# Kernel tuning notes

Hardware: AMD Instinct MI355X
Metric: run time of the kernel (lower is better)

Reference implementation:

```python
import jax, jax.numpy as jnp
import numpy as np

BASIS_SIZE = 256          # levels of the bitfield code
R_MAX = 1.0               # quantization range for normalized weights
QMAX = BASIS_SIZE // 2 - 1  # 127 -> symmetric int8-style grid
EPS = 1e-8


def setup_inputs() -> dict:
    key = jax.random.key(0)
    kx, kw, kb = jax.random.split(key, 3)
    B, S, D_IN, D_OUT = 4, 2048, 4096, 4096
    x = jax.random.normal(kx, (B, S, D_IN), dtype=jnp.float32)
    W = jax.random.normal(kw, (D_OUT, D_IN), dtype=jnp.float32)
    bias = jax.random.normal(kb, (D_OUT,), dtype=jnp.float32)
    return {"x": x, "W": W, "bias": bias}


def _bitfield_dequant_weight(W):
    # per-output-row L2 norm (p=2, dim=1 in torch)
    weight_norms = jnp.sqrt(jnp.sum(W * W, axis=1))          # [out]
    W_normalized = W / (weight_norms[:, None] + EPS)          # rows ~unit norm
    # bitfield encode/decode: uniform symmetric quantization to BASIS_SIZE
    # levels in [-R_MAX, R_MAX]
    scale = R_MAX / QMAX
    Wq = jnp.round(jnp.clip(W_normalized, -R_MAX, R_MAX) / scale) * scale
    return Wq, weight_norms


def reference(x, W, bias):
    Wq, weight_norms = _bitfield_dequant_weight(W)
    B, S, D_IN = x.shape
    x2 = x.reshape(-1, D_IN)                                  # [B*S, in]
    # bitfield matmul on normalized weights
    out_norm = jnp.einsum('nd,od->no', x2, Wq)                # [B*S, out]
    # denormalize (restore row norms) + bias epilogue
    out = out_norm * weight_norms
    out = out.reshape(B, S, -1) + bias
    return out
```

## Files before the change

### kernel.cpp

```cpp
#include <hip/hip_runtime.h>
#include <hip/hip_bf16.h>

typedef __attribute__((ext_vector_type(4))) int i32x4;
typedef __attribute__((address_space(3))) char lds3;

#define D_IN  4096
#define D_OUT 4096
#define M_TOT 8192
#define RSTRIDE ((size_t)64 * D_IN)

__device__ __forceinline__ void async16(const void* g, lds3* l) {
  __builtin_amdgcn_global_load_lds(
      (__attribute__((address_space(1))) void*)g,
      (__attribute__((address_space(3))) void*)l,
      16, 0, 0);
}

#define DSR(dst, addr, off) \
  asm volatile("ds_read_b128 %0, %1 offset:%2" : "=v"(dst) : "v"(addr), "i"(off))

__device__ __forceinline__ int pack4(float a, float b, float c, float d, float s) {
  int q0 = (int)rintf(a * s) & 255;
  int q1 = (int)rintf(b * s) & 255;
  int q2 = (int)rintf(c * s) & 255;
  int q3 = (int)rintf(d * s) & 255;
  return q0 | (q1 << 8) | (q2 << 16) | (q3 << 24);
}

__global__ void quant_x_kernel(const float* __restrict__ x, int4* __restrict__ xq,
                               float* __restrict__ sx) {
  const int row = blockIdx.x;
  const int t = threadIdx.x;
  const float* xr = x + (size_t)row * D_IN;

  float4 v[4];
  float mx = 0.f;
#pragma unroll
  for (int j = 0; j < 4; j++) {
    v[j] = ((const float4*)xr)[t * 4 + j];
    mx = fmaxf(mx, fmaxf(fmaxf(fabsf(v[j].x), fabsf(v[j].y)),
                         fmaxf(fabsf(v[j].z), fabsf(v[j].w))));
  }
#pragma unroll
  for (int off = 32; off; off >>= 1) mx = fmaxf(mx, __shfl_down(mx, off));
  __shared__ float red[4];
  __shared__ float smx;
  if ((t & 63) == 0) red[t >> 6] = mx;
  __syncthreads();
  if (t == 0) {
    float m = fmaxf(fmaxf(red[0], red[1]), fmaxf(red[2], red[3]));
    smx = m;
    sx[row] = m * (1.0f / 127.0f);
  }
  __syncthreads();

  const float inv = 127.0f / smx;
  int4 o;
  o.x = pack4(v[0].x, v[0].y, v[0].z, v[0].w, inv);
  o.y = pack4(v[1].x, v[1].y, v[1].z, v[1].w, inv);
  o.z = pack4(v[2].x, v[2].y, v[2].z, v[2].w, inv);
  o.w = pack4(v[3].x, v[3].y, v[3].z, v[3].w, inv);
  xq[(size_t)row * (D_IN / 16) + t] = o;
}

__global__ void quant_w_kernel(const float* __restrict__ W, int4* __restrict__ wq,
                               float* __restrict__ sn) {
  const int row = blockIdx.x;
  const int t = threadIdx.x;
  const float* wr = W + (size_t)row * D_IN;

  float4 v[4];
  double ss = 0.0;
#pragma unroll
  for (int j = 0; j < 4; j++) {
    v[j] = ((const float4*)wr)[t * 4 + j];
    ss += (double)v[j].x * v[j].x + (double)v[j].y * v[j].y +
          (double)v[j].z * v[j].z + (double)v[j].w * v[j].w;
  }
#pragma unroll
  for (int off = 32; off; off >>= 1) ss += __shfl_down(ss, off);
  __shared__ double red[4];
  __shared__ float shn;
  if ((t & 63) == 0) red[t >> 6] = ss;
  __syncthreads();
  if (t == 0) {
    double tot = red[0] + red[1] + red[2] + red[3];
    float nrm = (float)sqrt(tot);
    shn = nrm;
    sn[row] = nrm * (1.0f / 127.0f);
  }
  __syncthreads();

  const float den = shn + 1e-8f;
  int4 o;
  int* op = (int*)&o;
#pragma unroll
  for (int j = 0; j < 4; j++) {
    float e[4] = {v[j].x, v[j].y, v[j].z, v[j].w};
    int q[4];
#pragma unroll
    for (int c = 0; c < 4; c++) {
      float wn = e[c] / den;
      wn = fminf(1.0f, fmaxf(-1.0f, wn));
      q[c] = (int)rintf(wn * 127.0f) & 255;
    }
    op[j] = q[0] | (q[1] << 8) | (q[2] << 16) | (q[3] << 24);
  }
  wq[(size_t)row * (D_IN / 16) + t] = o;
}

template<int S, int VM, bool ISSUE>
__device__ __forceinline__ void k_iter(unsigned aA, unsigned aB,
                                       const char* pA, const char* pB,
                                       lds3* lA, lds3* lB,
                                       i32x4 (&acc)[4][4]) {
  asm volatile("s_waitcnt vmcnt(%0)" :: "i"(VM));
  asm volatile("s_barrier" ::: "memory");
  if (ISSUE) {
    async16(pA, lA);
    async16(pA + RSTRIDE, lA + 4096);
    async16(pB, lB);
    async16(pB + RSTRIDE, lB + 4096);
  }
  i32x4 af[4], bf[4];
  DSR(af[0], aA, S * 16384 + 0);
  DSR(af[1], aA, S * 16384 + 1024);
  DSR(af[2], aA, S * 16384 + 2048);
  DSR(af[3], aA, S * 16384 + 3072);
  DSR(bf[0], aB, S * 16384 + 8192 + 0);
  DSR(bf[1], aB, S * 16384 + 8192 + 1024);
  DSR(bf[2], aB, S * 16384 + 8192 + 2048);
  DSR(bf[3], aB, S * 16384 + 8192 + 3072);
  asm volatile("s_waitcnt lgkmcnt(0)"
               : "+v"(af[0]), "+v"(af[1]), "+v"(af[2]), "+v"(af[3]),
                 "+v"(bf[0]), "+v"(bf[1]), "+v"(bf[2]), "+v"(bf[3]));
#pragma unroll
  for (int mi = 0; mi < 4; mi++)
#pragma unroll
    for (int ni = 0; ni < 4; ni++)
      acc[mi][ni] = __builtin_amdgcn_mfma_i32_16x16x64_i8(af[mi], bf[ni], acc[mi][ni], 0, 0, 0);
}

__global__ __launch_bounds__(256, 3)
void gemm_i8_kernel(const char* __restrict__ A, const char* __restrict__ B,
                    const float* __restrict__ sx, const float* __restrict__ sn,
                    const float* __restrict__ bias, float* __restrict__ C) {
  __shared__ __align__(16) char smem[3 * 16384];

  const int t = threadIdx.x;
  const int lane = t & 63;
  const int wave = t >> 6;
  const int wm = wave >> 1, wn = wave & 1;
  const int m0 = blockIdx.y * 128;
  const int n0 = blockIdx.x * 128;

  const int srow = t >> 2;
  const int q = ((t & 3) - ((srow & 15) >> 1)) & 3;
  const char* gA = A + (size_t)(m0 + srow) * D_IN + q * 16;
  const char* gB = B + (size_t)(n0 + srow) * D_IN + q * 16;

  lds3* l3 = (lds3*)smem;
  lds3* lA0 = l3 + t * 16;
  lds3* lB0 = l3 + 8192 + t * 16;

  const int ml = lane & 15;
  const int g = lane >> 4;
  const unsigned cperm = (unsigned)((g + (ml >> 1)) & 3);
  const unsigned lds_base = (unsigned)(size_t)l3;
  const unsigned aA = lds_base + (wm * 64 + ml) * 64 + cperm * 16;
  const unsigned aB = lds_base + (wn * 64 + ml) * 64 + cperm * 16;

  i32x4 acc[4][4];
#pragma unroll
  for (int i = 0; i < 4; i++)
#pragma unroll
    for (int j = 0; j < 4; j++) acc[i][j] = (i32x4)0;

  async16(gA, lA0);            async16(gA + RSTRIDE, lA0 + 4096);
  async16(gB, lB0);            async16(gB + RSTRIDE, lB0 + 4096);
  async16(gA + 64, lA0 + 16384);           async16(gA + 64 + RSTRIDE, lA0 + 16384 + 4096);
  async16(gB + 64, lB0 + 16384);           async16(gB + 64 + RSTRIDE, lB0 + 16384 + 4096);

  const char* pA = gA + 128;
  const char* pB = gB + 128;

#pragma unroll 1
  for (int tr = 0; tr < 20; ++tr) {
    k_iter<0, 4, true>(aA, aB, pA, pB, lA0 + 32768, lB0 + 32768, acc); pA += 64; pB += 64;
    k_iter<1, 4, true>(aA, aB, pA, pB, lA0,         lB0,         acc); pA += 64; pB += 64;
    k_iter<2, 4, true>(aA, aB, pA, pB, lA0 + 16384, lB0 + 16384, acc); pA += 64; pB += 64;
  }
  k_iter<0, 4, true >(aA, aB, pA, pB, lA0 + 32768, lB0 + 32768, acc); pA += 64; pB += 64;
  k_iter<1, 4, true >(aA, aB, pA, pB, lA0,         lB0,         acc);
  k_iter<2, 4, false>(aA, aB, pA, pB, lA0,         lB0,         acc);
  k_iter<0, 0, false>(aA, aB, pA, pB, lA0,         lB0,         acc);

  float scn[4], bsv[4];
#pragma unroll
  for (int ni = 0; ni < 4; ni++) {
    const int col = n0 + wn * 64 + ni * 16 + ml;
    scn[ni] = sn[col];
    bsv[ni] = bias[col];
  }
#pragma unroll
  for (int mi = 0; mi < 4; mi++) {
    const int rbase = m0 + wm * 64 + mi * 16 + g * 4;
    float sxv[4];
#pragma unroll
    for (int r = 0; r < 4; r++) sxv[r] = sx[rbase + r];
#pragma unroll
    for (int ni = 0; ni < 4; ni++) {
      const int col = n0 + wn * 64 + ni * 16 + ml;
#pragma unroll
      for (int r = 0; r < 4; r++)
        C[(size_t)(rbase + r) * D_OUT + col] =
            (float)acc[mi][ni][r] * (sxv[r] * scn[ni]) + bsv[ni];
    }
  }
}

extern "C" void kernel_launch(void* const* d_in, const int* in_sizes, int n_in,
                              void* d_out, int out_size, void* d_ws, size_t ws_size,
                              hipStream_t stream) {
  const float* x    = (const float*)d_in[0];
  const float* W    = (const float*)d_in[1];
  const float* bias = (const float*)d_in[2];
  float* out = (float*)d_out;

  char* ws = (char*)d_ws;
  char*  xq = ws;
  char*  wq = ws + (size_t)M_TOT * D_IN;
  float* sx = (float*)(wq + (size_t)D_OUT * D_IN);
  float* sn = sx + M_TOT;

  quant_x_kernel<<<M_TOT, 256, 0, stream>>>(x, (int4*)xq, sx);
  quant_w_kernel<<<D_OUT, 256, 0, stream>>>(W, (int4*)wq, sn);
  dim3 grid(D_OUT / 128, M_TOT / 128);
  gemm_i8_kernel<<<grid, 256, 0, stream>>>(xq, wq, sx, sn, bias, out);
}
```

Baseline: 406.2 us.

## Software-pipeline LDS fragment reads with MFMA and use one wave per quant row

The int8 GEMM main loop now double-buffers register fragments. LDS reads for the next k-slice are issued before the MFMAs for the current slice, with sched_barriers and setprio used to keep that order and raise MFMA priority. This aims to hide ds_read latency behind the matrix cores, at the cost of more VGPRs, which may pressure occupancy under launch_bounds(256,3). The quantization kernels now give each 64-lane wave one row with coalesced loads and a shuffle-only reduction, removing the shared memory and __syncthreads barriers.

```diff
diff --git a/kernel.cpp b/kernel.cpp
--- a/kernel.cpp
+++ b/kernel.cpp
@@ -27,75 +27,54 @@
   return q0 | (q1 << 8) | (q2 << 16) | (q3 << 24);
 }
 
-__global__ void quant_x_kernel(const float* __restrict__ x, int4* __restrict__ xq,
+__global__ void quant_x_kernel(const float* __restrict__ x, int* __restrict__ xq,
                                float* __restrict__ sx) {
-  const int row = blockIdx.x;
-  const int t = threadIdx.x;
-  const float* xr = x + (size_t)row * D_IN;
-
-  float4 v[4];
+  const int row = blockIdx.x * 4 + (threadIdx.x >> 6);
+  const int lane = threadIdx.x & 63;
+  const float4* xr = (const float4*)(x + (size_t)row * D_IN);
+
+  float4 v[16];
   float mx = 0.f;
 #pragma unroll
-  for (int j = 0; j < 4; j++) {
-    v[j] = ((const float4*)xr)[t * 4 + j];
+  for (int j = 0; j < 16; j++) {
+    v[j] = xr[j * 64 + lane];
     mx = fmaxf(mx, fmaxf(fmaxf(fabsf(v[j].x), fabsf(v[j].y)),
                          fmaxf(fabsf(v[j].z), fabsf(v[j].w))));
   }
 #pragma unroll
-  for (int off = 32; off; off >>= 1) mx = fmaxf(mx, __shfl_down(mx, off));
-  __shared__ float red[4];
-  __shared__ float smx;
-  if ((t & 63) == 0) red[t >> 6] = mx;
-  __syncthreads();
-  if (t == 0) {
-    float m = fmaxf(fmaxf(red[0], red[1]), fmaxf(red[2], red[3]));
-    smx = m;
-    sx[row] = m * (1.0f / 127.0f);
-  }
-  __syncthreads();
-
-  const float inv = 127.0f / smx;
-  int4 o;
-  o.x = pack4(v[0].x, v[0].y, v[0].z, v[0].w, inv);
-  o.y = pack4(v[1].x, v[1].y, v[1].z, v[1].w, inv);
-  o.z = pack4(v[2].x, v[2].y, v[2].z, v[2].w, inv);
-  o.w = pack4(v[3].x, v[3].y, v[3].z, v[3].w, inv);
-  xq[(size_t)row * (D_IN / 16) + t] = o;
-}
-
-__global__ void quant_w_kernel(const float* __restrict__ W, int4* __restrict__ wq,
+  for (int off = 32; off; off >>= 1) mx = fmaxf(mx, __shfl_xor(mx, off));
+  if (lane == 0) sx[row] = mx * (1.0f / 127.0f);
+
+  const float inv = 127.0f / mx;
+  int* xqr = xq + (size_t)row * (D_IN / 4);
+#pragma unroll
+  for (int j = 0; j < 16; j++)
+    xqr[j * 64 + lane] = pack4(v[j].x, v[j].y, v[j].z, v[j].w, inv);
+}
+
+__global__ void quant_w_kernel(const float* __restrict__ W, int* __restrict__ wq,
                                float* __restrict__ sn) {
-  const int row = blockIdx.x;
-  const int t = threadIdx.x;
-  const float* wr = W + (size_t)row * D_IN;
-
-  float4 v[4];
+  const int row = blockIdx.x * 4 + (threadIdx.x >> 6);
+  const int lane = threadIdx.x & 63;
+  const float4* wr = (const float4*)(W + (size_t)row * D_IN);
+
+  float4 v[16];
   double ss = 0.0;
 #pragma unroll
-  for (int j = 0; j < 4; j++) {
-    v[j] = ((const float4*)wr)[t * 4 + j];
+  for (int j = 0; j < 16; j++) {
+    v[j] = wr[j * 64 + lane];
     ss += (double)v[j].x * v[j].x + (double)v[j].y * v[j].y +
           (double)v[j].z * v[j].z + (double)v[j].w * v[j].w;
   }
 #pragma unroll
-  for (int off = 32; off; off >>= 1) ss += __shfl_down(ss, off);
-  __shared__ double red[4];
-  __shared__ float shn;
-  if ((t & 63) == 0) red[t >> 6] = ss;
-  __syncthreads();
-  if (t == 0) {
-    double tot = red[0] + red[1] + red[2] + red[3];
-    float nrm = (float)sqrt(tot);
-    shn = nrm;
-    sn[row] = nrm * (1.0f / 127.0f);
-  }
-  __syncthreads();
-
-  const float den = shn + 1e-8f;
-  int4 o;
-  int* op = (int*)&o;
-#pragma unroll
-  for (int j = 0; j < 4; j++) {
+  for (int off = 32; off; off >>= 1) ss += __shfl_xor(ss, off);
+  const float nrm = (float)sqrt(ss);
+  if (lane == 0) sn[row] = nrm * (1.0f / 127.0f);
+
+  const float den = nrm + 1e-8f;
+  int* wqr = wq + (size_t)row * (D_IN / 4);
+#pragma unroll
+  for (int j = 0; j < 16; j++) {
     float e[4] = {v[j].x, v[j].y, v[j].z, v[j].w};
     int q[4];
 #pragma unroll
@@ -104,41 +83,47 @@
       wn = fminf(1.0f, fmaxf(-1.0f, wn));
       q[c] = (int)rintf(wn * 127.0f) & 255;
     }
-    op[j] = q[0] | (q[1] << 8) | (q[2] << 16) | (q[3] << 24);
-  }
-  wq[(size_t)row * (D_IN / 16) + t] = o;
-}
-
-template<int S, int VM, bool ISSUE>
-__device__ __forceinline__ void k_iter(unsigned aA, unsigned aB,
-                                       const char* pA, const char* pB,
-                                       lds3* lA, lds3* lB,
+    wqr[j * 64 + lane] = q[0] | (q[1] << 8) | (q[2] << 16) | (q[3] << 24);
+  }
+}
+
+template<int S, int VM, bool ISSUE, bool MF>
+__device__ __forceinline__ void k_pipe(unsigned aA, unsigned aB,
+                                       const char*& pA, const char*& pB,
+                                       lds3* lA0, lds3* lB0,
+                                       i32x4 (&fill)[8], i32x4 (&use)[8],
                                        i32x4 (&acc)[4][4]) {
   asm volatile("s_waitcnt vmcnt(%0)" :: "i"(VM));
   asm volatile("s_barrier" ::: "memory");
   if (ISSUE) {
-    async16(pA, lA);
-    async16(pA + RSTRIDE, lA + 4096);
-    async16(pB, lB);
-    async16(pB + RSTRIDE, lB + 4096);
-  }
-  i32x4 af[4], bf[4];
-  DSR(af[0], aA, S * 16384 + 0);
-  DSR(af[1], aA, S * 16384 + 1024);
-  DSR(af[2], aA, S * 16384 + 2048);
-  DSR(af[3], aA, S * 16384 + 3072);
-  DSR(bf[0], aB, S * 16384 + 8192 + 0);
-  DSR(bf[1], aB, S * 16384 + 8192 + 1024);
-  DSR(bf[2], aB, S * 16384 + 8192 + 2048);
-  DSR(bf[3], aB, S * 16384 + 8192 + 3072);
+    constexpr int T = ((S + 2) % 3) * 16384;
+    async16(pA, lA0 + T);  async16(pA + RSTRIDE, lA0 + T + 4096);
+    async16(pB, lB0 + T);  async16(pB + RSTRIDE, lB0 + T + 4096);
+    pA += 64; pB += 64;
+  }
+  DSR(fill[0], aA, S * 16384 + 0);
+  DSR(fill[1], aA, S * 16384 + 1024);
+  DSR(fill[2], aA, S * 16384 + 2048);
+  DSR(fill[3], aA, S * 16384 + 3072);
+  DSR(fill[4], aB, S * 16384 + 8192 + 0);
+  DSR(fill[5], aB, S * 16384 + 8192 + 1024);
+  DSR(fill[6], aB, S * 16384 + 8192 + 2048);
+  DSR(fill[7], aB, S * 16384 + 8192 + 3072);
+  __builtin_amdgcn_sched_barrier(0);
+  if (MF) {
+    __builtin_amdgcn_s_setprio(1);
+#pragma unroll
+    for (int mi = 0; mi < 4; mi++)
+#pragma unroll
+      for (int ni = 0; ni < 4; ni++)
+        acc[mi][ni] = __builtin_amdgcn_mfma_i32_16x16x64_i8(use[mi], use[4 + ni],
+                                                            acc[mi][ni], 0, 0, 0);
+    __builtin_amdgcn_s_setprio(0);
+  }
+  __builtin_amdgcn_sched_barrier(0);
   asm volatile("s_waitcnt lgkmcnt(0)"
-               : "+v"(af[0]), "+v"(af[1]), "+v"(af[2]), "+v"(af[3]),
-                 "+v"(bf[0]), "+v"(bf[1]), "+v"(bf[2]), "+v"(bf[3]));
-#pragma unroll
-  for (int mi = 0; mi < 4; mi++)
-#pragma unroll
-    for (int ni = 0; ni < 4; ni++)
-      acc[mi][ni] = __builtin_amdgcn_mfma_i32_16x16x64_i8(af[mi], bf[ni], acc[mi][ni], 0, 0, 0);
+               : "+v"(fill[0]), "+v"(fill[1]), "+v"(fill[2]), "+v"(fill[3]),
+                 "+v"(fill[4]), "+v"(fill[5]), "+v"(fill[6]), "+v"(fill[7]));
 }
 
 __global__ __launch_bounds__(256, 3)
@@ -176,6 +161,8 @@
 #pragma unroll
     for (int j = 0; j < 4; j++) acc[i][j] = (i32x4)0;
 
+  i32x4 fA[8], fB[8];
+
   async16(gA, lA0);            async16(gA + RSTRIDE, lA0 + 4096);
   async16(gB, lB0);            async16(gB + RSTRIDE, lB0 + 4096);
   async16(gA + 64, lA0 + 16384);           async16(gA + 64 + RSTRIDE, lA0 + 16384 + 4096);
@@ -184,16 +171,32 @@
   const char* pA = gA + 128;
   const char* pB = gB + 128;
 
+  k_pipe<0, 4, true, false>(aA, aB, pA, pB, lA0, lB0, fA, fB, acc);
+  k_pipe<1, 4, true, true >(aA, aB, pA, pB, lA0, lB0, fB, fA, acc);
+  k_pipe<2, 4, true, true >(aA, aB, pA, pB, lA0, lB0, fA, fB, acc);
+  k_pipe<0, 4, true, true >(aA, aB, pA, pB, lA0, lB0, fB, fA, acc);
+  k_pipe<1, 4, true, true >(aA, aB, pA, pB, lA0, lB0, fA, fB, acc);
+  k_pipe<2, 4, true, true >(aA, aB, pA, pB, lA0, lB0, fB, fA, acc);
+
 #pragma unroll 1
-  for (int tr = 0; tr < 20; ++tr) {
-    k_iter<0, 4, true>(aA, aB, pA, pB, lA0 + 32768, lB0 + 32768, acc); pA += 64; pB += 64;
-    k_iter<1, 4, true>(aA, aB, pA, pB, lA0,         lB0,         acc); pA += 64; pB += 64;
-    k_iter<2, 4, true>(aA, aB, pA, pB, lA0 + 16384, lB0 + 16384, acc); pA += 64; pB += 64;
-  }
-  k_iter<0, 4, true >(aA, aB, pA, pB, lA0 + 32768, lB0 + 32768, acc); pA += 64; pB += 64;
-  k_iter<1, 4, true >(aA, aB, pA, pB, lA0,         lB0,         acc);
-  k_iter<2, 4, false>(aA, aB, pA, pB, lA0,         lB0,         acc);
-  k_iter<0, 0, false>(aA, aB, pA, pB, lA0,         lB0,         acc);
+  for (int tr = 0; tr < 9; ++tr) {
+    k_pipe<0, 4, true, true>(aA, aB, pA, pB, lA0, lB0, fA, fB, acc);
+    k_pipe<1, 4, true, true>(aA, aB, pA, pB, lA0, lB0, fB, fA, acc);
+    k_pipe<2, 4, true, true>(aA, aB, pA, pB, lA0, lB0, fA, fB, acc);
+    k_pipe<0, 4, true, true>(aA, aB, pA, pB, lA0, lB0, fB, fA, acc);
+    k_pipe<1, 4, true, true>(aA, aB, pA, pB, lA0, lB0, fA, fB, acc);
+    k_pipe<2, 4, true, true>(aA, aB, pA, pB, lA0, lB0, fB, fA, acc);
+  }
+  k_pipe<0, 4, true,  true>(aA, aB, pA, pB, lA0, lB0, fA, fB, acc);
+  k_pipe<1, 4, true,  true>(aA, aB, pA, pB, lA0, lB0, fB, fA, acc);
+  k_pipe<2, 4, false, true>(aA, aB, pA, pB, lA0, lB0, fA, fB, acc);
+  k_pipe<0, 0, false, true>(aA, aB, pA, pB, lA0, lB0, fB, fA, acc);
+#pragma unroll
+  for (int mi = 0; mi < 4; mi++)
+#pragma unroll
+    for (int ni = 0; ni < 4; ni++)
+      acc[mi][ni] = __builtin_amdgcn_mfma_i32_16x16x64_i8(fB[mi], fB[4 + ni],
+                                                          acc[mi][ni], 0, 0, 0);
 
   float scn[4], bsv[4];
 #pragma unroll
@@ -233,8 +236,8 @@
   float* sx = (float*)(wq + (size_t)D_OUT * D_IN);
   float* sn = sx + M_TOT;
 
-  quant_x_kernel<<<M_TOT, 256, 0, stream>>>(x, (int4*)xq, sx);
-  quant_w_kernel<<<D_OUT, 256, 0, stream>>>(W, (int4*)wq, sn);
+  quant_x_kernel<<<M_TOT / 4, 256, 0, stream>>>(x, (int*)xq, sx);
+  quant_w_kernel<<<D_OUT / 4, 256, 0, stream>>>(W, (int*)wq, sn);
   dim3 grid(D_OUT / 128, M_TOT / 128);
   gemm_i8_kernel<<<grid, 256, 0, stream>>>(xq, wq, sx, sn, bias, out);
 }
```

Result: slower. 426.0 us (+4.9%).
